# Optimization experiments

Measured on AMD Instinct MI355X. Metric: run time of the kernel, lower is better.

Reference implementation:

```python
import jax, jax.numpy as jnp
import numpy as np

N_NODES = 50000
N_EDGES = 800000
NODE_DIM = 128
EDGE_DIM = 2
HID = 512
SLOPE = 0.15  # LeakyReLU negative slope


def _leaky(x):
    return jnp.where(x > 0, x, SLOPE * x)


def _lin(key, fan_in, fan_out, bias=True):
    s = 1.0 / np.sqrt(fan_in)
    k1, k2 = jax.random.split(key)
    W = jax.random.uniform(k1, (fan_in, fan_out), jnp.float32, -s, s)
    if not bias:
        return W
    b = jax.random.uniform(k2, (fan_out,), jnp.float32, -s, s)
    return W, b


def setup_inputs() -> dict:
    key = jax.random.key(0)
    ks = jax.random.split(key, 12)
    x = jax.random.normal(ks[0], (N_NODES, NODE_DIM), jnp.float32)
    edge_index = jax.random.randint(ks[1], (2, N_EDGES), 0, N_NODES, jnp.int32)
    edge_attr = jax.random.normal(ks[2], (N_EDGES, EDGE_DIM), jnp.float32)
    We, be = _lin(ks[3], EDGE_DIM, HID)
    # SAGEConv: out = lin_l(mean_agg(x_j)) + lin_r(x_i); lin_l has bias, lin_r does not
    W1l, b1 = _lin(ks[4], NODE_DIM, HID)
    W1r = _lin(ks[5], NODE_DIM, HID, bias=False)
    W2l, b2 = _lin(ks[6], HID, 256)
    W2r = _lin(ks[7], HID, 256, bias=False)
    W3l, b3 = _lin(ks[8], 256, 64)
    W3r = _lin(ks[9], 256, 64, bias=False)
    Wp, bp = _lin(ks[10], 64, 32)
    kf1, kf2 = jax.random.split(ks[11])
    Wf1, bf1 = _lin(kf1, 32, 32)
    Wf2, bf2 = _lin(kf2, 32, 2)
    return dict(x=x, edge_index=edge_index, edge_attr=edge_attr,
                We=We, be=be, W1l=W1l, b1=b1, W1r=W1r,
                W2l=W2l, b2=b2, W2r=W2r, W3l=W3l, b3=b3, W3r=W3r,
                Wp=Wp, bp=bp, Wf1=Wf1, bf1=bf1, Wf2=Wf2, bf2=bf2)


def _sage(h, src, dst, Wl, bl, Wr):
    # mean aggregation of source-node features at destination nodes
    n = h.shape[0]
    summed = jax.ops.segment_sum(h[src], dst, num_segments=n)          # [N, d]
    cnt = jax.ops.segment_sum(jnp.ones((src.shape[0],), h.dtype), dst, num_segments=n)
    mean = summed / jnp.maximum(cnt, 1.0)[:, None]
    return mean @ Wl + bl + h @ Wr


def reference(x, edge_index, edge_attr, We, be, W1l, b1, W1r,
              W2l, b2, W2r, W3l, b3, W3r, Wp, bp, Wf1, bf1, Wf2, bf2):
    src, dst = edge_index[0], edge_index[1]
    _edge_feats = edge_attr @ We + be  # computed in the original forward but never used downstream
    h = _leaky(_sage(x, src, dst, W1l, b1, W1r))   # dropout is identity in eval
    h = _leaky(_sage(h, src, dst, W2l, b2, W2r))
    h = _leaky(_sage(h, src, dst, W3l, b3, W3r))
    h = h @ Wp + bp                                 # pre_fc
    h = _leaky(h @ Wf1 + bf1)                       # classifier (Linear fallback)
    return h @ Wf2 + bf2                            # [N, 2]
```

## Files before the change

### kernel.cpp

```cpp
#include <hip/hip_runtime.h>
#include <hip/hip_fp16.h>

#define N_NODES 50000
#define N_EDGES 800000
#define SLOPE 0.15f

typedef unsigned short u16;
typedef __attribute__((ext_vector_type(8))) _Float16 f16x8;
typedef __attribute__((ext_vector_type(4))) float f32x4;

static __device__ __forceinline__ float leaky(float v) { return v > 0.f ? v : SLOPE * v; }

static __device__ __forceinline__ u16 f2h(float v) {
    return __builtin_bit_cast(u16, __float2half(v));
}

static __device__ __forceinline__ void async_load16(const u16* g, u16* l) {
    __builtin_amdgcn_global_load_lds(
        (const __attribute__((address_space(1))) unsigned int*)g,
        (__attribute__((address_space(3))) unsigned int*)l, 16, 0, 0);
}

__global__ void k_prep(const int* __restrict__ dst, int* __restrict__ cnt,
                       const float* __restrict__ x, u16* __restrict__ xp,
                       const float* __restrict__ W1l, const float* __restrict__ W1r,
                       const float* __restrict__ W2l, const float* __restrict__ W2r,
                       const float* __restrict__ W3l, const float* __restrict__ W3r,
                       u16* w1lp, u16* w1rp, u16* w2cp, u16* w3cp) {
    int b = blockIdx.x, tid = threadIdx.x;
    if (b < 3125) {
        int e = b * 256 + tid;
        if (e < N_EDGES) atomicAdd(&cnt[dst[e]], 1);
        return;
    }
    b -= 3125;
    if (b < 6250) {
        int i = b * 256 + tid;
        if (i >= N_NODES * 32) return;
        float4 v = ((const float4*)x)[i];
        ((ushort4*)xp)[i] = make_ushort4(f2h(v.x), f2h(v.y), f2h(v.z), f2h(v.w));
        return;
    }
    b -= 6250;
    const float* W; u16* op; int K, N;
    if (b < 256)       { W = W1l; op = w1lp; K = 128; N = 512; }
    else if (b < 512)  { W = W1r; op = w1rp; K = 128; N = 512; b -= 256; }
    else if (b < 1024) { W = W2l; op = w2cp; K = 512; N = 256; b -= 512; }
    else if (b < 1536) { W = W2r; op = w2cp + 256 * 512; K = 512; N = 256; b -= 1024; }
    else if (b < 1600) { W = W3l; op = w3cp; K = 256; N = 64; b -= 1536; }
    else               { W = W3r; op = w3cp + 64 * 256; K = 256; N = 64; b -= 1600; }
    int i = b * 256 + tid;
    if (i >= K * N) return;
    int k = i / N, n = i - k * N;
    op[(size_t)n * K + k] = f2h(W[i]);
}

__global__ __launch_bounds__(1024) void k_scan1(const int* __restrict__ cnt,
                                                int* __restrict__ offs,
                                                int* __restrict__ bsum) {
    __shared__ int wsum[16];
    int tid = threadIdx.x, lane = tid & 63, wv = tid >> 6;
    int i = blockIdx.x * 1024 + tid;
    int orig = (i < N_NODES) ? cnt[i] : 0;
    int v = orig;
#pragma unroll
    for (int d = 1; d < 64; d <<= 1) {
        int t = __shfl_up(v, d, 64);
        if (lane >= d) v += t;
    }
    if (lane == 63) wsum[wv] = v;
    __syncthreads();
    if (wv == 0) {
        int s = (lane < 16) ? wsum[lane] : 0;
#pragma unroll
        for (int d = 1; d < 16; d <<= 1) {
            int t = __shfl_up(s, d, 64);
            if (lane >= d) s += t;
        }
        if (lane < 16) wsum[lane] = s;
        if (lane == 15) bsum[blockIdx.x] = s;
    }
    __syncthreads();
    int wpre = (wv == 0) ? 0 : wsum[wv - 1];
    if (i < N_NODES) offs[i] = v + wpre - orig;
}

__global__ void k_scan3(const int* __restrict__ cnt, int* __restrict__ offs,
                        int* __restrict__ cursor, float* __restrict__ inv,
                        const int* __restrict__ bsum, int nb) {
    __shared__ int sb[64];
    int tid = threadIdx.x;
    if (tid < 64) {
        int v = (tid < nb) ? bsum[tid] : 0;
        int s = v;
#pragma unroll
        for (int d = 1; d < 64; d <<= 1) {
            int t = __shfl_up(s, d, 64);
            if (tid >= d) s += t;
        }
        sb[tid] = s - v;
    }
    __syncthreads();
    int i = blockIdx.x * 256 + tid;
    if (i >= N_NODES) return;
    int c = cnt[i];
    int o = offs[i] + sb[i >> 10];
    offs[i] = o;
    cursor[i] = o;
    inv[i] = 1.0f / (float)(c > 1 ? c : 1);
    if (i == 0) offs[N_NODES] = N_EDGES;
}

__global__ void k_fill(const int* __restrict__ src, const int* __restrict__ dst,
                       int* __restrict__ cursor, int* __restrict__ ssrc) {
    int e = blockIdx.x * 256 + threadIdx.x;
    if (e < N_EDGES) {
        int pos = atomicAdd(&cursor[dst[e]], 1);
        ssrc[pos] = src[e];
    }
}

template <int STRIDE, int EPI>
__global__ __launch_bounds__(256) void k_aggf(const u16* __restrict__ tbl,
                                              const int* __restrict__ offs,
                                              const int* __restrict__ ssrc,
                                              const float* __restrict__ inv,
                                              const u16* __restrict__ y,
                                              const float* __restrict__ bias,
                                              u16* __restrict__ outh,
                                              float* __restrict__ outf) {
    constexpr int U = 4;
    int wid = (blockIdx.x * 256 + threadIdx.x) >> 6;
    if (wid >= N_NODES) return;
    const int coff = blockIdx.y * 64;
    int lane = threadIdx.x & 63;
    int eg = lane >> 3;
    int cl = lane & 7;
    int beg = offs[wid], end = offs[wid + 1];
    float acc[8] = {};
    for (int e = beg + eg; e < end; e += U * 8) {
        int idx[U]; float msk[U];
#pragma unroll
        for (int j = 0; j < U; ++j) {
            int ee = e + j * 8;
            bool ok = ee < end;
            idx[j] = ssrc[ok ? ee : e];
            msk[j] = ok ? 1.f : 0.f;
        }
#pragma unroll
        for (int j = 0; j < U; ++j) {
            uint4 rv = *(const uint4*)(tbl + (size_t)idx[j] * STRIDE + coff + cl * 8);
            const __half2* hp = (const __half2*)&rv;
#pragma unroll
            for (int t = 0; t < 4; ++t) {
                float2 f = __half22float2(hp[t]);
                acc[t * 2 + 0] = fmaf(f.x, msk[j], acc[t * 2 + 0]);
                acc[t * 2 + 1] = fmaf(f.y, msk[j], acc[t * 2 + 1]);
            }
        }
    }
#pragma unroll
    for (int m = 8; m < 64; m <<= 1)
#pragma unroll
        for (int t = 0; t < 8; ++t) acc[t] += __shfl_xor(acc[t], m, 64);
    if (eg != 0) return;
    float wv = inv[wid];
    const size_t ob = (size_t)wid * STRIDE + coff + cl * 8;
    float v[8];
    if (EPI == 0) {
#pragma unroll
        for (int t = 0; t < 8; ++t) v[t] = acc[t] * wv;
    } else {
        uint4 yv4 = *(const uint4*)(y + ob);
        const __half2* yp = (const __half2*)&yv4;
        float4 b0 = *(const float4*)(bias + coff + cl * 8);
        float4 b1 = *(const float4*)(bias + coff + cl * 8 + 4);
        float bb[8] = {b0.x, b0.y, b0.z, b0.w, b1.x, b1.y, b1.z, b1.w};
#pragma unroll
        for (int t = 0; t < 4; ++t) {
            float2 f = __half22float2(yp[t]);
            v[t * 2 + 0] = leaky(acc[t * 2 + 0] * wv + f.x + bb[t * 2 + 0]);
            v[t * 2 + 1] = leaky(acc[t * 2 + 1] * wv + f.y + bb[t * 2 + 1]);
        }
    }
    if (EPI == 3) {
        *(float4*)(outf + ob)     = make_float4(v[0], v[1], v[2], v[3]);
        *(float4*)(outf + ob + 4) = make_float4(v[4], v[5], v[6], v[7]);
    } else {
        *(ushort4*)(outh + ob)     = make_ushort4(f2h(v[0]), f2h(v[1]), f2h(v[2]), f2h(v[3]));
        *(ushort4*)(outh + ob + 4) = make_ushort4(f2h(v[4]), f2h(v[5]), f2h(v[6]), f2h(v[7]));
    }
}

__global__ __launch_bounds__(256, 4) void k_gemm_f(
    int M, int nct,
    const u16* __restrict__ A1, const u16* __restrict__ B1, int K1,
    const u16* __restrict__ A2, const u16* __restrict__ B2, int K2,
    const float* __restrict__ bias, int act, int colsplit,
    u16* __restrict__ out1h, int n1, u16* __restrict__ out2h, int n2) {
    __shared__ u16 Ash[4096], Bsh[4096];
    const int tid = threadIdx.x;
    const int lane = tid & 63;
    const int w = tid >> 6;
    const int wm = w & 1, wn = w >> 1;
    const int fr = lane & 15;
    const int q = lane >> 4;

    const int mT = (M + 127) >> 7;
    const int lin = blockIdx.x;
    const int grp = lin / (8 * nct);
    const int idx = lin - grp * (8 * nct);
    const int ct = idx >> 3;
    const int s8 = idx & 7;
    const int rowt = grp * 8 + s8;
    if (rowt >= mT) return;
    const int brow = rowt * 128;
    const int bcol = ct * 128;

    const int T1 = K1 >> 5, T = T1 + (K2 >> 5);

    const int c0 = (w * 2 + 0) * 64 + lane;
    const int c1 = (w * 2 + 1) * 64 + lane;
    const int r0 = c0 >> 2, g0 = (c0 & 3) ^ ((r0 >> 1) & 3);
    const int r1 = c1 >> 2, g1 = (c1 & 3) ^ ((r1 >> 1) & 3);
    int ar0 = brow + r0; if (ar0 >= M) ar0 = M - 1;
    int ar1 = brow + r1; if (ar1 >= M) ar1 = M - 1;
    const int br0 = bcol + r0, br1 = bcol + r1;
    const int ub0 = (w * 2 + 0) * 512;
    const int ub1 = (w * 2 + 1) * 512;

    f32x4 acc[4][4] = {};

    for (int kt = 0; kt < T; ++kt) {
        const u16 *A, *B; int K, k0;
        if (kt < T1) { A = A1; B = B1; K = K1; k0 = kt * 32; }
        else         { A = A2; B = B2; K = K2; k0 = (kt - T1) * 32; }
        __syncthreads();
        {
            size_t ga0 = (size_t)ar0 * K + k0 + g0 * 8;
            size_t ga1 = (size_t)ar1 * K + k0 + g1 * 8;
            size_t gb0 = (size_t)br0 * K + k0 + g0 * 8;
            size_t gb1 = (size_t)br1 * K + k0 + g1 * 8;
            async_load16(A + ga0, &Ash[ub0]);
            async_load16(A + ga1, &Ash[ub1]);
            async_load16(B + gb0, &Bsh[ub0]);
            async_load16(B + gb1, &Bsh[ub1]);
        }
        __syncthreads();
        f16x8 fa[4], fb[4];
#pragma unroll
        for (int rt = 0; rt < 4; ++rt) {
            int row = wm * 64 + rt * 16 + fr;
            int ad = row * 32 + ((q ^ ((row >> 1) & 3)) * 8);
            fa[rt] = __builtin_bit_cast(f16x8, *(const uint4*)&Ash[ad]);
        }
#pragma unroll
        for (int ctf = 0; ctf < 4; ++ctf) {
            int row = wn * 64 + ctf * 16 + fr;
            int ad = row * 32 + ((q ^ ((row >> 1) & 3)) * 8);
            fb[ctf] = __builtin_bit_cast(f16x8, *(const uint4*)&Bsh[ad]);
        }
#pragma unroll
        for (int rt = 0; rt < 4; ++rt)
#pragma unroll
            for (int ctf = 0; ctf < 4; ++ctf)
                acc[rt][ctf] = __builtin_amdgcn_mfma_f32_16x16x32_f16(fa[rt], fb[ctf], acc[rt][ctf], 0, 0, 0);
    }

#pragma unroll
    for (int rt = 0; rt < 4; ++rt) {
        int rowb = brow + wm * 64 + rt * 16 + q * 4;
#pragma unroll
        for (int ctf = 0; ctf < 4; ++ctf) {
            int col = bcol + wn * 64 + ctf * 16 + fr;
            float b = bias ? bias[col] : 0.f;
#pragma unroll
            for (int r = 0; r < 4; ++r) {
                int row = rowb + r;
                if (row >= M) continue;
                float v = acc[rt][ctf][r] + b;
                if (act) v = leaky(v);
                if (col < colsplit) out1h[(size_t)row * n1 + col] = f2h(v);
                else                out2h[(size_t)row * n2 + (col - colsplit)] = f2h(v);
            }
        }
    }
}

__global__ __launch_bounds__(256) void k_head(const float* __restrict__ h3,
                                              const float* __restrict__ Wp, const float* __restrict__ bp,
                                              const float* __restrict__ Wf1, const float* __restrict__ bf1,
                                              const float* __restrict__ Wf2, const float* __restrict__ bf2,
                                              float* __restrict__ out) {
    __shared__ float sWp[64 * 32], sW1[32 * 32], sW2[32 * 2];
    __shared__ float sbp[32], sb1[32], sb2[2];
    int tid = threadIdx.x;
    for (int i = tid; i < 64 * 32; i += 256) sWp[i] = Wp[i];
    for (int i = tid; i < 32 * 32; i += 256) sW1[i] = Wf1[i];
    for (int i = tid; i < 64; i += 256) sW2[i] = Wf2[i];
    if (tid < 32) { sbp[tid] = bp[tid]; sb1[tid] = bf1[tid]; }
    if (tid < 2) sb2[tid] = bf2[tid];
    __syncthreads();
    int row = blockIdx.x * 256 + tid;
    if (row >= N_NODES) return;
    const float4* h4v = (const float4*)(h3 + (size_t)row * 64);
    float xr[64];
#pragma unroll
    for (int i = 0; i < 16; ++i) {
        float4 v = h4v[i];
        xr[i * 4 + 0] = v.x; xr[i * 4 + 1] = v.y;
        xr[i * 4 + 2] = v.z; xr[i * 4 + 3] = v.w;
    }
    float h4[32];
    for (int o = 0; o < 32; ++o) {
        float s = sbp[o];
#pragma unroll
        for (int i = 0; i < 64; ++i) s += xr[i] * sWp[i * 32 + o];
        h4[o] = s;
    }
    float h5[32];
    for (int o = 0; o < 32; ++o) {
        float s = sb1[o];
#pragma unroll
        for (int i = 0; i < 32; ++i) s += h4[i] * sW1[i * 32 + o];
        h5[o] = leaky(s);
    }
#pragma unroll
    for (int o = 0; o < 2; ++o) {
        float s = sb2[o];
#pragma unroll
        for (int i = 0; i < 32; ++i) s += h5[i] * sW2[i * 2 + o];
        out[(size_t)row * 2 + o] = s;
    }
}

extern "C" void kernel_launch(void* const* d_in, const int* in_sizes, int n_in,
                              void* d_out, int out_size, void* d_ws, size_t ws_size,
                              hipStream_t stream) {
    const float* x   = (const float*)d_in[0];
    const int*   ei  = (const int*)d_in[1];
    const float* W1l = (const float*)d_in[5];
    const float* b1  = (const float*)d_in[6];
    const float* W1r = (const float*)d_in[7];
    const float* W2l = (const float*)d_in[8];
    const float* b2  = (const float*)d_in[9];
    const float* W2r = (const float*)d_in[10];
    const float* W3l = (const float*)d_in[11];
    const float* b3  = (const float*)d_in[12];
    const float* W3r = (const float*)d_in[13];
    const float* Wp  = (const float*)d_in[14];
    const float* bp  = (const float*)d_in[15];
    const float* Wf1 = (const float*)d_in[16];
    const float* bf1 = (const float*)d_in[17];
    const float* Wf2 = (const float*)d_in[18];
    const float* bf2 = (const float*)d_in[19];
    float* out = (float*)d_out;
    (void)in_sizes; (void)n_in; (void)out_size; (void)ws_size;

    const int* src = ei;
    const int* dst = ei + N_EDGES;

    char* base = (char*)d_ws;
    size_t off = 0;
    auto alloc = [&](size_t bytes) -> void* {
        void* r = base + off;
        off = (off + bytes + 255) & ~(size_t)255;
        return r;
    };
    const size_t NN = N_NODES;
    int*   cnt    = (int*)alloc(NN * 4);
    int*   offs   = (int*)alloc((NN + 1) * 4);
    int*   cursor = (int*)alloc(NN * 4);
    float* inv    = (float*)alloc(NN * 4);
    int*   bsum   = (int*)alloc(64 * 4);
    int*   ssrc   = (int*)alloc((size_t)N_EDGES * 4);
    u16* w1lp = (u16*)alloc(128 * 512 * 2);
    u16* w1rp = (u16*)alloc(128 * 512 * 2);
    u16* w2cp = (u16*)alloc(512 * 512 * 2);
    u16* w3cp = (u16*)alloc(128 * 256 * 2);
    u16* xp  = (u16*)alloc(NN * 128 * 2);
    u16* axp = (u16*)alloc(NN * 128 * 2);
    u16* h1p = (u16*)alloc(NN * 512 * 2);
    u16* z2h = (u16*)alloc(NN * 256 * 2);
    u16* y2h = (u16*)alloc(NN * 256 * 2);
    u16* h2p = (u16*)alloc(NN * 256 * 2);
    u16* z3h = (u16*)alloc(NN * 64 * 2);
    u16* y3h = (u16*)alloc(NN * 64 * 2);
    float* h3f = (float*)alloc(NN * 64 * 4);

    hipMemsetAsync(cnt, 0, NN * 4, stream);
    k_prep<<<3125 + 6250 + 1664, 256, 0, stream>>>(dst, cnt, x, xp,
        W1l, W1r, W2l, W2r, W3l, W3r, w1lp, w1rp, w2cp, w3cp);
    const int nb = (N_NODES + 1023) / 1024;
    k_scan1<<<nb, 1024, 0, stream>>>(cnt, offs, bsum);
    k_scan3<<<(N_NODES + 255) / 256, 256, 0, stream>>>(cnt, offs, cursor, inv, bsum, nb);
    k_fill<<<(N_EDGES + 255) / 256, 256, 0, stream>>>(src, dst, cursor, ssrc);

    const int aggGrid = (N_NODES + 3) / 4;
    const int mT = (N_NODES + 127) / 128;
    const int grid4 = ((mT + 7) / 8) * 32;
    const int grid1 = ((mT + 7) / 8) * 8;

    k_aggf<128, 0><<<dim3(aggGrid, 2), 256, 0, stream>>>(
        xp, offs, ssrc, inv, nullptr, nullptr, axp, nullptr);
    k_gemm_f<<<grid4, 256, 0, stream>>>(N_NODES, 4,
        axp, w1lp, 128, xp, w1rp, 128, b1, 1, 512, h1p, 512, nullptr, 0);

    k_gemm_f<<<grid4, 256, 0, stream>>>(N_NODES, 4,
        h1p, w2cp, 512, nullptr, nullptr, 0, nullptr, 0, 256, z2h, 256, y2h, 256);
    k_aggf<256, 2><<<dim3(aggGrid, 4), 256, 0, stream>>>(
        z2h, offs, ssrc, inv, y2h, b2, h2p, nullptr);

    k_gemm_f<<<grid1, 256, 0, stream>>>(N_NODES, 1,
        h2p, w3cp, 256, nullptr, nullptr, 0, nullptr, 0, 64, z3h, 64, y3h, 64);
    k_aggf<64, 3><<<dim3(aggGrid, 1), 256, 0, stream>>>(
        z3h, offs, ssrc, inv, y3h, b3, nullptr, h3f);

    k_head<<<(N_NODES + 255) / 256, 256, 0, stream>>>(h3f,
        Wp, bp, Wf1, bf1, Wf2, bf2, out);
}
```

Measured before the change: 464.0 us.

## Pad CSR segments to multiples of 16 and vectorize aggregation gathers

Rounds each node's CSR segment up to a multiple of 16 and fills the pad slots with a sentinel index that points at an extra zeroed row of each feature table. This removes bounds masking and allows vector index loads. The aggregation kernel now covers the full feature width in one wave, so each index is read once rather than once per column block. It accumulates fp16 pairs with the fdot2 instruction after permuting halves. The cost is more index memory, up to 15 dummy gathers per node, and fp16 pair arithmetic inside fdot2.

```diff
diff --git a/kernel.cpp b/kernel.cpp
--- a/kernel.cpp
+++ b/kernel.cpp
@@ -7,12 +7,18 @@
 
 typedef unsigned short u16;
 typedef __attribute__((ext_vector_type(8))) _Float16 f16x8;
+typedef __attribute__((ext_vector_type(2))) _Float16 h16x2;
 typedef __attribute__((ext_vector_type(4))) float f32x4;
 
 static __device__ __forceinline__ float leaky(float v) { return v > 0.f ? v : SLOPE * v; }
 
 static __device__ __forceinline__ u16 f2h(float v) {
     return __builtin_bit_cast(u16, __float2half(v));
+}
+
+static __device__ __forceinline__ float dot2acc(unsigned int u, float c) {
+    h16x2 one = {(_Float16)1.0f, (_Float16)1.0f};
+    return __builtin_amdgcn_fdot2(__builtin_bit_cast(h16x2, u), one, c, false);
 }
 
 static __device__ __forceinline__ void async_load16(const u16* g, u16* l) {
@@ -61,7 +67,8 @@
     __shared__ int wsum[16];
     int tid = threadIdx.x, lane = tid & 63, wv = tid >> 6;
     int i = blockIdx.x * 1024 + tid;
-    int orig = (i < N_NODES) ? cnt[i] : 0;
+    int c = (i < N_NODES) ? cnt[i] : 0;
+    int orig = (c + 15) & ~15;
     int v = orig;
 #pragma unroll
     for (int d = 1; d < 64; d <<= 1) {
@@ -99,6 +106,7 @@
             if (tid >= d) s += t;
         }
         sb[tid] = s - v;
+        if (blockIdx.x == 0 && tid == nb - 1) offs[N_NODES] = s;
     }
     __syncthreads();
     int i = blockIdx.x * 256 + tid;
@@ -108,73 +116,83 @@
     offs[i] = o;
     cursor[i] = o;
     inv[i] = 1.0f / (float)(c > 1 ? c : 1);
-    if (i == 0) offs[N_NODES] = N_EDGES;
 }
 
 __global__ void k_fill(const int* __restrict__ src, const int* __restrict__ dst,
-                       int* __restrict__ cursor, int* __restrict__ ssrc) {
+                       int* __restrict__ cursor, int* __restrict__ pssrc,
+                       const int* __restrict__ poffs, const int* __restrict__ cnt) {
     int e = blockIdx.x * 256 + threadIdx.x;
     if (e < N_EDGES) {
         int pos = atomicAdd(&cursor[dst[e]], 1);
-        ssrc[pos] = src[e];
-    }
-}
-
-template <int STRIDE, int EPI>
-__global__ __launch_bounds__(256) void k_aggf(const u16* __restrict__ tbl,
-                                              const int* __restrict__ offs,
-                                              const int* __restrict__ ssrc,
-                                              const float* __restrict__ inv,
-                                              const u16* __restrict__ y,
-                                              const float* __restrict__ bias,
-                                              u16* __restrict__ outh,
-                                              float* __restrict__ outf) {
-    constexpr int U = 4;
+        pssrc[pos] = src[e];
+    } else {
+        int t = e - N_EDGES;
+        int i = t >> 4, j = t & 15;
+        int pos = poffs[i] + cnt[i] + j;
+        if (pos < poffs[i + 1]) pssrc[pos] = N_NODES;
+    }
+}
+
+template <int STRIDE, int EPI, int LPE, int U>
+__global__ __launch_bounds__(256) void k_agg(const u16* __restrict__ tbl,
+                                             const int* __restrict__ poffs,
+                                             const int* __restrict__ pssrc,
+                                             const float* __restrict__ inv,
+                                             const u16* __restrict__ y,
+                                             const float* __restrict__ bias,
+                                             u16* __restrict__ outh,
+                                             float* __restrict__ outf) {
+    constexpr int G = 64 / LPE;
     int wid = (blockIdx.x * 256 + threadIdx.x) >> 6;
     if (wid >= N_NODES) return;
-    const int coff = blockIdx.y * 64;
     int lane = threadIdx.x & 63;
-    int eg = lane >> 3;
-    int cl = lane & 7;
-    int beg = offs[wid], end = offs[wid + 1];
+    int g = lane / LPE;
+    int cl = lane % LPE;
+    int beg = poffs[wid], end = poffs[wid + 1];
+    const u16* colbase = tbl + cl * 8;
     float acc[8] = {};
-    for (int e = beg + eg; e < end; e += U * 8) {
-        int idx[U]; float msk[U];
-#pragma unroll
-        for (int j = 0; j < U; ++j) {
-            int ee = e + j * 8;
-            bool ok = ee < end;
-            idx[j] = ssrc[ok ? ee : e];
-            msk[j] = ok ? 1.f : 0.f;
-        }
-#pragma unroll
-        for (int j = 0; j < U; ++j) {
-            uint4 rv = *(const uint4*)(tbl + (size_t)idx[j] * STRIDE + coff + cl * 8);
-            const __half2* hp = (const __half2*)&rv;
+    for (int e = beg + g * U; e < end; e += G * U) {
+        int idx[U];
+        if constexpr (U == 4) {
+            int4 t4 = *(const int4*)&pssrc[e];
+            idx[0] = t4.x; idx[1] = t4.y; idx[2] = t4.z; idx[3] = t4.w;
+        } else {
+            int2 t2 = *(const int2*)&pssrc[e];
+            idx[0] = t2.x; idx[1] = t2.y;
+        }
+        uint4 rv[U];
+#pragma unroll
+        for (int j = 0; j < U; ++j)
+            rv[j] = *(const uint4*)(colbase + (size_t)idx[j] * STRIDE);
+#pragma unroll
+        for (int p = 0; p < U / 2; ++p) {
+            const unsigned int* a = (const unsigned int*)&rv[2 * p];
+            const unsigned int* b = (const unsigned int*)&rv[2 * p + 1];
 #pragma unroll
             for (int t = 0; t < 4; ++t) {
-                float2 f = __half22float2(hp[t]);
-                acc[t * 2 + 0] = fmaf(f.x, msk[j], acc[t * 2 + 0]);
-                acc[t * 2 + 1] = fmaf(f.y, msk[j], acc[t * 2 + 1]);
+                unsigned int lo = __builtin_amdgcn_perm(b[t], a[t], 0x05040100u);
+                unsigned int hi = __builtin_amdgcn_perm(b[t], a[t], 0x07060302u);
+                acc[2 * t + 0] = dot2acc(lo, acc[2 * t + 0]);
+                acc[2 * t + 1] = dot2acc(hi, acc[2 * t + 1]);
             }
         }
     }
 #pragma unroll
-    for (int m = 8; m < 64; m <<= 1)
+    for (int m = LPE; m < 64; m <<= 1)
 #pragma unroll
         for (int t = 0; t < 8; ++t) acc[t] += __shfl_xor(acc[t], m, 64);
-    if (eg != 0) return;
+    if (g != 0) return;
     float wv = inv[wid];
-    const size_t ob = (size_t)wid * STRIDE + coff + cl * 8;
+    const size_t ob = (size_t)wid * STRIDE + cl * 8;
     float v[8];
-    if (EPI == 0) {
+    if constexpr (EPI == 0) {
 #pragma unroll
         for (int t = 0; t < 8; ++t) v[t] = acc[t] * wv;
     } else {
         uint4 yv4 = *(const uint4*)(y + ob);
         const __half2* yp = (const __half2*)&yv4;
-        float4 b0 = *(const float4*)(bias + coff + cl * 8);
-        float4 b1 = *(const float4*)(bias + coff + cl * 8 + 4);
+        float4 b0 = *(const float4*)(bias + cl * 8);
+        float4 b1 = *(const float4*)(bias + cl * 8 + 4);
         float bb[8] = {b0.x, b0.y, b0.z, b0.w, b1.x, b1.y, b1.z, b1.w};
 #pragma unroll
         for (int t = 0; t < 4; ++t) {
@@ -183,7 +201,7 @@
             v[t * 2 + 1] = leaky(acc[t * 2 + 1] * wv + f.y + bb[t * 2 + 1]);
         }
     }
-    if (EPI == 3) {
+    if constexpr (EPI == 3) {
         *(float4*)(outf + ob)     = make_float4(v[0], v[1], v[2], v[3]);
         *(float4*)(outf + ob + 4) = make_float4(v[4], v[5], v[6], v[7]);
     } else {
@@ -373,48 +391,52 @@
     int*   cursor = (int*)alloc(NN * 4);
     float* inv    = (float*)alloc(NN * 4);
     int*   bsum   = (int*)alloc(64 * 4);
-    int*   ssrc   = (int*)alloc((size_t)N_EDGES * 4);
+    int*   pssrc  = (int*)alloc((size_t)(N_EDGES + 16 * N_NODES) * 4);
     u16* w1lp = (u16*)alloc(128 * 512 * 2);
     u16* w1rp = (u16*)alloc(128 * 512 * 2);
     u16* w2cp = (u16*)alloc(512 * 512 * 2);
     u16* w3cp = (u16*)alloc(128 * 256 * 2);
-    u16* xp  = (u16*)alloc(NN * 128 * 2);
+    u16* xp  = (u16*)alloc((NN + 1) * 128 * 2);
     u16* axp = (u16*)alloc(NN * 128 * 2);
     u16* h1p = (u16*)alloc(NN * 512 * 2);
-    u16* z2h = (u16*)alloc(NN * 256 * 2);
+    u16* z2h = (u16*)alloc((NN + 1) * 256 * 2);
     u16* y2h = (u16*)alloc(NN * 256 * 2);
     u16* h2p = (u16*)alloc(NN * 256 * 2);
-    u16* z3h = (u16*)alloc(NN * 64 * 2);
+    u16* z3h = (u16*)alloc((NN + 1) * 64 * 2);
     u16* y3h = (u16*)alloc(NN * 64 * 2);
     float* h3f = (float*)alloc(NN * 64 * 4);
 
     hipMemsetAsync(cnt, 0, NN * 4, stream);
+    hipMemsetAsync(xp + NN * 128, 0, 128 * 2, stream);
+    hipMemsetAsync(z2h + NN * 256, 0, 256 * 2, stream);
+    hipMemsetAsync(z3h + NN * 64, 0, 64 * 2, stream);
     k_prep<<<3125 + 6250 + 1664, 256, 0, stream>>>(dst, cnt, x, xp,
         W1l, W1r, W2l, W2r, W3l, W3r, w1lp, w1rp, w2cp, w3cp);
     const int nb = (N_NODES + 1023) / 1024;
     k_scan1<<<nb, 1024, 0, stream>>>(cnt, offs, bsum);
     k_scan3<<<(N_NODES + 255) / 256, 256, 0, stream>>>(cnt, offs, cursor, inv, bsum, nb);
-    k_fill<<<(N_EDGES + 255) / 256, 256, 0, stream>>>(src, dst, cursor, ssrc);
+    k_fill<<<(N_EDGES + 16 * N_NODES + 255) / 256, 256, 0, stream>>>(
+        src, dst, cursor, pssrc, offs, cnt);
 
     const int aggGrid = (N_NODES + 3) / 4;
     const int mT = (N_NODES + 127) / 128;
     const int grid4 = ((mT + 7) / 8) * 32;
     const int grid1 = ((mT + 7) / 8) * 8;
 
-    k_aggf<128, 0><<<dim3(aggGrid, 2), 256, 0, stream>>>(
-        xp, offs, ssrc, inv, nullptr, nullptr, axp, nullptr);
+    k_agg<128, 0, 16, 4><<<aggGrid, 256, 0, stream>>>(
+        xp, offs, pssrc, inv, nullptr, nullptr, axp, nullptr);
     k_gemm_f<<<grid4, 256, 0, stream>>>(N_NODES, 4,
         axp, w1lp, 128, xp, w1rp, 128, b1, 1, 512, h1p, 512, nullptr, 0);
 
     k_gemm_f<<<grid4, 256, 0, stream>>>(N_NODES, 4,
         h1p, w2cp, 512, nullptr, nullptr, 0, nullptr, 0, 256, z2h, 256, y2h, 256);
-    k_aggf<256, 2><<<dim3(aggGrid, 4), 256, 0, stream>>>(
-        z2h, offs, ssrc, inv, y2h, b2, h2p, nullptr);
+    k_agg<256, 2, 32, 4><<<aggGrid, 256, 0, stream>>>(
+        z2h, offs, pssrc, inv, y2h, b2, h2p, nullptr);
 
     k_gemm_f<<<grid1, 256, 0, stream>>>(N_NODES, 1,
         h2p, w3cp, 256, nullptr, nullptr, 0, nullptr, 0, 64, z3h, 64, y3h, 64);
-    k_aggf<64, 3><<<dim3(aggGrid, 1), 256, 0, stream>>>(
-        z3h, offs, ssrc, inv, y3h, b3, nullptr, h3f);
+    k_agg<64, 3, 8, 2><<<aggGrid, 256, 0, stream>>>(
+        z3h, offs, pssrc, inv, y3h, b3, nullptr, h3f);
 
     k_head<<<(N_NODES + 255) / 256, 256, 0, stream>>>(h3f,
         Wp, bp, Wf1, bf1, Wf2, bf2, out);
```

New measurement: 471.3 us. Within noise of the previous version (+1.6%).
